# Kernel optimization log

Hardware: AMD Instinct MI355X
Metric: run time of the kernel (lower is better)

Reference implementation:

```python
import jax, jax.numpy as jnp
import numpy as np

N_BINS = 10  # module default n_bins


def setup_inputs() -> dict:
    key = jax.random.key(0)
    k1, k2 = jax.random.split(key)
    N, C = 1_000_000, 64
    logits = jax.random.normal(k1, (N, C), dtype=jnp.float32)
    labels = jax.random.randint(k2, (N,), 0, C)
    return {"logits": logits, "labels": labels, "train": 1}


def _ece_from_conf(confidences, correctness, n_bins):
    # bin i covers (i/n_bins, (i+1)/n_bins]; conf > 1/C > 0 after softmax so
    # ceil(conf*n_bins)-1 reproduces the gt(lower)*le(upper) masking.
    bin_idx = jnp.clip(jnp.ceil(confidences * n_bins).astype(jnp.int32) - 1, 0, n_bins - 1)
    ones = jnp.ones_like(confidences)
    counts = jax.ops.segment_sum(ones, bin_idx, num_segments=n_bins)
    conf_sum = jax.ops.segment_sum(confidences, bin_idx, num_segments=n_bins)
    corr_sum = jax.ops.segment_sum(correctness.astype(confidences.dtype), bin_idx, num_segments=n_bins)
    n_total = confidences.shape[0]
    safe = jnp.maximum(counts, 1.0)
    per_bin = jnp.abs(conf_sum / safe - corr_sum / safe) * (counts / n_total)
    ece = jnp.sum(jnp.where(counts > 0, per_bin, 0.0))
    return ece.reshape(1)


def reference(logits, labels, train):
    # train is a static Python int, so this branch resolves at trace time.
    if train:
        softmaxes = jax.nn.softmax(logits, axis=1)
        confidences = jnp.max(softmaxes, axis=1)
        predictions = jnp.argmax(softmaxes, axis=1)
    else:
        softmaxes = jax.nn.softmax(logits, axis=0)
        predictions = jnp.argmax(softmaxes, axis=0)
        t = 1e-05  # smooth-max over classes via tempered logsumexp
        confidences = t * jax.scipy.special.logsumexp(softmaxes / t, axis=0)
    correctness = predictions == labels
    return _ece_from_conf(confidences, correctness, N_BINS)
```

## Files before the change

### kernel.cpp

```cpp
#include <hip/hip_runtime.h>
#include <hip/hip_bf16.h>


#define N_BINS 10
#define C 64

#define WS_COUNTER_OFF 30

__global__ void ece_init_ws(double* ws) {
    int t = threadIdx.x;
    if (t < 3 * N_BINS) ws[t] = 0.0;
    if (t == 0) *(unsigned int*)(ws + WS_COUNTER_OFF) = 0u;
}

__device__ __forceinline__ void row_reduce(const float4 v, float& conf, int& idx) {
    float m = v.x; int mi = 0;
    if (v.y > m) { m = v.y; mi = 1; }
    if (v.z > m) { m = v.z; mi = 2; }
    if (v.w > m) { m = v.w; mi = 3; }
    idx = ((threadIdx.x & 15) << 2) + mi;
    #pragma unroll
    for (int off = 1; off < 16; off <<= 1) {
        float om = __shfl_xor(m, off, 64);
        int   oi = __shfl_xor(idx, off, 64);
        if (om > m || (om == m && oi < idx)) { m = om; idx = oi; }
    }
    float se = __expf(v.x - m) + __expf(v.y - m) + __expf(v.z - m) + __expf(v.w - m);
    #pragma unroll
    for (int off = 1; off < 16; off <<= 1) se += __shfl_xor(se, off, 64);
    conf = 1.0f / se;
}

__global__ __launch_bounds__(256) void ece_main(const float* __restrict__ logits,
                                                const int* __restrict__ labels,
                                                double* __restrict__ gbins,
                                                float* __restrict__ out,
                                                int N) {
    __shared__ float s_cnt[N_BINS];
    __shared__ float s_conf[N_BINS];
    __shared__ float s_corr[N_BINS];
    __shared__ int s_last;
    const int tid = threadIdx.x;
    if (tid < N_BINS) {
        s_cnt[tid] = 0.0f;
        s_conf[tid] = 0.0f;
        s_corr[tid] = 0.0f;
    }
    __syncthreads();

    const int lane16 = tid & 15;
    const int group0 = (blockIdx.x * blockDim.x + tid) >> 4;
    const int ngroups = (gridDim.x * blockDim.x) >> 4;

    for (int row = group0; row < N; row += 2 * ngroups) {
        const int row2 = row + ngroups;
        const float4 v1 = reinterpret_cast<const float4*>(logits + (size_t)row * C)[lane16];
        float4 v2;
        if (row2 < N) v2 = reinterpret_cast<const float4*>(logits + (size_t)row2 * C)[lane16];

        float conf1; int idx1;
        row_reduce(v1, conf1, idx1);
        float conf2 = 0.0f; int idx2 = 0;
        if (row2 < N) row_reduce(v2, conf2, idx2);

        if (lane16 == 0) {
            {
                int bin = min(max((int)ceilf(conf1 * (float)N_BINS) - 1, 0), N_BINS - 1);
                atomicAdd(&s_cnt[bin], 1.0f);
                atomicAdd(&s_conf[bin], conf1);
                if (idx1 == labels[row]) atomicAdd(&s_corr[bin], 1.0f);
            }
            if (row2 < N) {
                int bin = min(max((int)ceilf(conf2 * (float)N_BINS) - 1, 0), N_BINS - 1);
                atomicAdd(&s_cnt[bin], 1.0f);
                atomicAdd(&s_conf[bin], conf2);
                if (idx2 == labels[row2]) atomicAdd(&s_corr[bin], 1.0f);
            }
        }
    }
    __syncthreads();
    if (tid < N_BINS) {
        if (s_cnt[tid] != 0.0f) {
            atomicAdd(&gbins[tid], (double)s_cnt[tid]);
            atomicAdd(&gbins[N_BINS + tid], (double)s_conf[tid]);
            atomicAdd(&gbins[2 * N_BINS + tid], (double)s_corr[tid]);
        }
    }

    if (tid == 0) {
        __threadfence();
        unsigned int old = atomicAdd((unsigned int*)(gbins + WS_COUNTER_OFF), 1u);
        s_last = (old == gridDim.x - 1) ? 1 : 0;
    }
    __syncthreads();
    if (s_last && tid == 0) {
        __threadfence();
        double ece = 0.0;
        for (int b = 0; b < N_BINS; ++b) {
            double cnt = atomicAdd(&gbins[b], 0.0);
            if (cnt > 0.0) {
                double conf = atomicAdd(&gbins[N_BINS + b], 0.0) / cnt;
                double corr = atomicAdd(&gbins[2 * N_BINS + b], 0.0) / cnt;
                double d = conf - corr;
                if (d < 0.0) d = -d;
                ece += d * (cnt / (double)N);
            }
        }
        out[0] = (float)ece;
    }
}

extern "C" void kernel_launch(void* const* d_in, const int* in_sizes, int n_in,
                              void* d_out, int out_size, void* d_ws, size_t ws_size,
                              hipStream_t stream) {
    const float* logits = (const float*)d_in[0];
    const int* labels = (const int*)d_in[1];
    float* out = (float*)d_out;
    double* gbins = (double*)d_ws;

    const int N = in_sizes[1];

    ece_init_ws<<<1, 64, 0, stream>>>(gbins);
    ece_main<<<2048, 256, 0, stream>>>(logits, labels, gbins, out, N);
}
```

Before: 418.8 us.

## Process one row per thread instead of sixteen lanes per row

Switches from a 16-lane group per row, which needed shuffle reductions for max and sum-exp, to one thread per row that loads all 64 logits into registers and reduces them serially. This removes the cross-lane shuffles and lets every lane do useful binning instead of one lane in sixteen. In exchange each thread reads a 256-byte row, so loads across a wavefront are strided by row and no longer coalesced. It also raises register pressure and makes LDS atomic contention much heavier, since every thread now issues its own atomics into the ten shared bins.

```diff
diff --git a/kernel.cpp b/kernel.cpp
--- a/kernel.cpp
+++ b/kernel.cpp
@@ -11,24 +11,6 @@
     int t = threadIdx.x;
     if (t < 3 * N_BINS) ws[t] = 0.0;
     if (t == 0) *(unsigned int*)(ws + WS_COUNTER_OFF) = 0u;
-}
-
-__device__ __forceinline__ void row_reduce(const float4 v, float& conf, int& idx) {
-    float m = v.x; int mi = 0;
-    if (v.y > m) { m = v.y; mi = 1; }
-    if (v.z > m) { m = v.z; mi = 2; }
-    if (v.w > m) { m = v.w; mi = 3; }
-    idx = ((threadIdx.x & 15) << 2) + mi;
-    #pragma unroll
-    for (int off = 1; off < 16; off <<= 1) {
-        float om = __shfl_xor(m, off, 64);
-        int   oi = __shfl_xor(idx, off, 64);
-        if (om > m || (om == m && oi < idx)) { m = om; idx = oi; }
-    }
-    float se = __expf(v.x - m) + __expf(v.y - m) + __expf(v.z - m) + __expf(v.w - m);
-    #pragma unroll
-    for (int off = 1; off < 16; off <<= 1) se += __shfl_xor(se, off, 64);
-    conf = 1.0f / se;
 }
 
 __global__ __launch_bounds__(256) void ece_main(const float* __restrict__ logits,
@@ -48,35 +30,48 @@
     }
     __syncthreads();
 
-    const int lane16 = tid & 15;
-    const int group0 = (blockIdx.x * blockDim.x + tid) >> 4;
-    const int ngroups = (gridDim.x * blockDim.x) >> 4;
+    const int gtid = blockIdx.x * blockDim.x + tid;
+    const int gstride = gridDim.x * blockDim.x;
 
-    for (int row = group0; row < N; row += 2 * ngroups) {
-        const int row2 = row + ngroups;
-        const float4 v1 = reinterpret_cast<const float4*>(logits + (size_t)row * C)[lane16];
-        float4 v2;
-        if (row2 < N) v2 = reinterpret_cast<const float4*>(logits + (size_t)row2 * C)[lane16];
+    for (int row = gtid; row < N; row += gstride) {
+        const float4* rp = reinterpret_cast<const float4*>(logits + (size_t)row * C);
+        const int lbl = labels[row];
 
-        float conf1; int idx1;
-        row_reduce(v1, conf1, idx1);
-        float conf2 = 0.0f; int idx2 = 0;
-        if (row2 < N) row_reduce(v2, conf2, idx2);
+        float4 q[16];
+        #pragma unroll
+        for (int j = 0; j < 16; ++j) q[j] = rp[j];
 
-        if (lane16 == 0) {
-            {
-                int bin = min(max((int)ceilf(conf1 * (float)N_BINS) - 1, 0), N_BINS - 1);
-                atomicAdd(&s_cnt[bin], 1.0f);
-                atomicAdd(&s_conf[bin], conf1);
-                if (idx1 == labels[row]) atomicAdd(&s_corr[bin], 1.0f);
-            }
-            if (row2 < N) {
-                int bin = min(max((int)ceilf(conf2 * (float)N_BINS) - 1, 0), N_BINS - 1);
-                atomicAdd(&s_cnt[bin], 1.0f);
-                atomicAdd(&s_conf[bin], conf2);
-                if (idx2 == labels[row2]) atomicAdd(&s_corr[bin], 1.0f);
-            }
+        float mx = q[0].x, my = q[0].y, mz = q[0].z, mw = q[0].w;
+        int ix = 0, iy = 0, iz = 0, iw = 0;
+        #pragma unroll
+        for (int j = 1; j < 16; ++j) {
+            if (q[j].x > mx) { mx = q[j].x; ix = j; }
+            if (q[j].y > my) { my = q[j].y; iy = j; }
+            if (q[j].z > mz) { mz = q[j].z; iz = j; }
+            if (q[j].w > mw) { mw = q[j].w; iw = j; }
         }
+        float m = mx; int idx = (ix << 2);
+        int cand = (iy << 2) | 1;
+        if (my > m || (my == m && cand < idx)) { m = my; idx = cand; }
+        cand = (iz << 2) | 2;
+        if (mz > m || (mz == m && cand < idx)) { m = mz; idx = cand; }
+        cand = (iw << 2) | 3;
+        if (mw > m || (mw == m && cand < idx)) { m = mw; idx = cand; }
+
+        float sx = 0.0f, sy = 0.0f, sz = 0.0f, sw = 0.0f;
+        #pragma unroll
+        for (int j = 0; j < 16; ++j) {
+            sx += __expf(q[j].x - m);
+            sy += __expf(q[j].y - m);
+            sz += __expf(q[j].z - m);
+            sw += __expf(q[j].w - m);
+        }
+        const float conf = 1.0f / ((sx + sy) + (sz + sw));
+
+        int bin = min(max((int)ceilf(conf * (float)N_BINS) - 1, 0), N_BINS - 1);
+        atomicAdd(&s_cnt[bin], 1.0f);
+        atomicAdd(&s_conf[bin], conf);
+        if (idx == lbl) atomicAdd(&s_corr[bin], 1.0f);
     }
     __syncthreads();
     if (tid < N_BINS) {
```

Measured after the change: 451.3 us. +7.8%, slower.
